# Performance work log

Measured on AMD Instinct MI355X. Metric: run time of the kernel, lower is better.

The kernel has to match this reference:

```python
import jax, jax.numpy as jnp
import numpy as np

H = 768   # config.hidden_size
B = 1024  # batch
S = 256   # attention context length
C1, C2, C3 = 202, 183, 11  # num_class for crit, law, time


def setup_inputs() -> dict:
    key = jax.random.key(0)
    ks = jax.random.split(key, 18)
    sd = 1.0 / np.sqrt(H)
    def u(k, shape):
        return jax.random.uniform(k, shape, jnp.float32, -sd, sd)
    return {
        "x": jax.random.normal(ks[0], (B, H), jnp.float32),
        "attn": jax.random.normal(ks[1], (B, S, H), jnp.float32),
        # 3 LSTMCells (tasks crit, law, time), stacked
        "Wih": u(ks[2], (3, 4 * H, H)),
        "Whh": u(ks[3], (3, 4 * H, H)),
        "bih": u(ks[4], (3, 4 * H)),
        "bhh": u(ks[5], (3, 4 * H)),
        # edge (2->3) hidden/cell state Linear (only edge whose FC is reached)
        "hfc_W": u(ks[6], (H, H)), "hfc_b": u(ks[7], (H,)),
        "cfc_W": u(ks[8], (H, H)), "cfc_b": u(ks[9], (H,)),
        # midfc per task
        "midfc_W": u(ks[10], (3, H, H)), "midfc_b": u(ks[11], (3, H)),
        # outfc per task (distinct class counts)
        "out1_W": u(ks[12], (C1, H)), "out1_b": u(ks[13], (C1,)),
        "out2_W": u(ks[14], (C2, H)), "out2_b": u(ks[15], (C2,)),
        "out3_W": u(ks[16], (C3, H)), "out3_b": u(ks[17], (C3,)),
    }


def _lstm_cell(x, h, c, Wih, Whh, bih, bhh):
    # torch nn.LSTMCell: gate order i, f, g, o
    gates = x @ Wih.T + bih + h @ Whh.T + bhh
    i, f, g, o = jnp.split(gates, 4, axis=-1)
    c_new = jax.nn.sigmoid(f) * c + jax.nn.sigmoid(i) * jnp.tanh(g)
    h_new = jax.nn.sigmoid(o) * jnp.tanh(c_new)
    return h_new, c_new


def _attend(h, attn):
    # Attention: ratio = softmax(bmm(attn, h)); result = bmm(attn^T, ratio)
    w = jax.nn.softmax(jnp.einsum('bsh,bh->bs', attn, h), axis=1)
    return jnp.einsum('bsh,bs->bh', attn, w)


def _head(h, mW, mb, oW, ob):
    # more_fc=True: outfc(relu(midfc(h)))
    return jax.nn.relu(h @ mW.T + mb) @ oW.T + ob


def reference(x, attn, Wih, Whh, bih, bhh, hfc_W, hfc_b, cfc_W, cfc_b,
              midfc_W, midfc_b, out1_W, out1_b, out2_W, out2_b, out3_W, out3_b):
    # graph "[(1 2),(1 3),(2 3)]": edges 1->2, 1->3, 2->3; initial hidden_list all zero.
    z = jnp.zeros_like(x)
    # task 1 (crit): runs on zero state; first-touch sets hidden[2]=hidden[3]=(h1,c1)
    h1, c1 = _lstm_cell(x, z, z, Wih[0], Whh[0], bih[0], bhh[0])
    # task 2 (law): state = (h1, c1)
    h2, c2 = _lstm_cell(x, h1, c1, Wih[1], Whh[1], bih[1], bhh[1])
    # edge 2->3 applies the per-edge Linear and accumulates into hidden[3]
    hp3 = h1 + h2 @ hfc_W.T + hfc_b
    cp3 = c1 + c2 @ cfc_W.T + cfc_b
    # task 3 (time)
    h3, c3 = _lstm_cell(x, hp3, cp3, Wih[2], Whh[2], bih[2], bhh[2])
    # attention over encoder context, per task head
    a1 = _attend(h1, attn)
    a2 = _attend(h2, attn)
    a3 = _attend(h3, attn)
    o1 = _head(a1, midfc_W[0], midfc_b[0], out1_W, out1_b)
    o2 = _head(a2, midfc_W[1], midfc_b[1], out2_W, out2_b)
    o3 = _head(a3, midfc_W[2], midfc_b[2], out3_W, out3_b)
    return (o1, o2, o3)
```

## Files before the change

kernel.cpp:

```cpp
#include <hip/hip_runtime.h>


typedef unsigned short u16;
typedef _Float16       f16x8 __attribute__((ext_vector_type(8)));
typedef float          f32x4 __attribute__((ext_vector_type(4)));

#define SWZ(r) ((((r) + ((r) >> 2))) & 3)
#define VMCNT(N) asm volatile("s_waitcnt vmcnt(" #N ")" ::: "memory")
#define KBAR()  do { __builtin_amdgcn_s_barrier(); __builtin_amdgcn_sched_barrier(0); } while (0)

__device__ __forceinline__ u16 f2h(float f) {
  _Float16 h = (_Float16)f;
  return __builtin_bit_cast(u16, h);
}
__device__ __forceinline__ float sigm(float x) { return 1.f / (1.f + __expf(-x)); }
__device__ __forceinline__ float ftanh(float x) { return 1.f - 2.f / (__expf(2.f * x) + 1.f); }

__device__ __forceinline__ void gld16(const u16* g, u16* l) {
  __builtin_amdgcn_global_load_lds(
      (const __attribute__((address_space(1))) unsigned int*)(g),
      (__attribute__((address_space(3))) unsigned int*)(l),
      16, 0, 0);
}

struct KP { const u16 *pA1, *pA2, *pW1_0, *pW2_0, *pW1_1, *pW2_1; };

__device__ __forceinline__ void stage_tile(const KP& kp, int kt, int ntA,
                                           u16* Asb, u16* Bsb, int wv) {
  const bool s1 = (kt < ntA);
  const int off = (s1 ? kt : kt - ntA) * 32;
  gld16((s1 ? kp.pA1  : kp.pA2 ) + off, Asb + wv * 512);
  gld16((s1 ? kp.pW1_0 : kp.pW2_0) + off, Bsb + wv * 512);
  gld16((s1 ? kp.pW1_1 : kp.pW2_1) + off, Bsb + 2048 + wv * 512);
}

__device__ __forceinline__ void compute_tile(const u16* Asb, const u16* Bsb,
                                             int wv, int frow, int fsl, f32x4* acc) {
  const int ar = wv * 16 + frow;
  f16x8 ah = *(const f16x8*)(Asb + ar * 32 + ((fsl ^ SWZ(ar)) * 8));
  f16x8 bh[8];
#pragma unroll
  for (int n = 0; n < 8; ++n) {
    const int br = n * 16 + frow;
    bh[n] = *(const f16x8*)(Bsb + br * 32 + ((fsl ^ SWZ(br)) * 8));
  }
#pragma unroll
  for (int n = 0; n < 8; ++n)
    acc[n] = __builtin_amdgcn_mfma_f32_16x16x32_f16(ah, bh[n], acc[n], 0, 0, 0);
}

#define KLOOP(kp, ntA, NT, As, Bs, wv, frow, fsl, acc)                          \
  do {                                                                          \
    stage_tile(kp, 0, ntA, As, Bs, wv);                                         \
    stage_tile(kp, 1, ntA, As + 2048, Bs + 4096, wv);                           \
    stage_tile(kp, 2, ntA, As + 4096, Bs + 8192, wv);                           \
    for (int t = 0; t < NT - 2; ++t) {                                          \
      VMCNT(6); KBAR();                                                         \
      const int cb = t & 3;                                                     \
      compute_tile(As + cb * 2048, Bs + cb * 4096, wv, frow, fsl, acc);         \
      if (t + 3 < NT) {                                                         \
        const int sb = (t + 3) & 3;                                             \
        stage_tile(kp, t + 3, ntA, As + sb * 2048, Bs + sb * 4096, wv);         \
      }                                                                         \
    }                                                                           \
    VMCNT(3); KBAR();                                                           \
    compute_tile(As + ((NT - 2) & 3) * 2048, Bs + ((NT - 2) & 3) * 4096,        \
                 wv, frow, fsl, acc);                                           \
    VMCNT(0); KBAR();                                                           \
    compute_tile(As + ((NT - 1) & 3) * 2048, Bs + ((NT - 1) & 3) * 4096,        \
                 wv, frow, fsl, acc);                                           \
  } while (0)

struct GJob {
  const u16* A; const u16* W;
  float* outf; u16* outh;
  const float* bias; const float* bias2; const float* addend;
  int N; int ldc; int relu;
};
struct GArgs { GJob j[3]; };

__global__ __launch_bounds__(256)
void gemm_k(GArgs P)
{
  const GJob jb = P.j[blockIdx.z];
  const int bn0 = blockIdx.x * 128;
  if (bn0 >= jb.N) return;
  const int bm0 = blockIdx.y * 64;

  __shared__ __align__(16) u16 As[4 * 64 * 32];
  __shared__ __align__(16) u16 Bs[4 * 128 * 32];

  const int tid = threadIdx.x, lane = tid & 63, wv = tid >> 6;
  const int frow = lane & 15, fsl = lane >> 4;

  const int ra  = tid >> 2,        csa  = (tid & 3) ^ SWZ(ra);
  const int rb0 = tid >> 2,        csb0 = (tid & 3) ^ SWZ(rb0);
  const int rb1 = (tid >> 2) + 64, csb1 = (tid & 3) ^ SWZ(rb1);
  int wr0 = bn0 + rb0; if (wr0 >= jb.N) wr0 = jb.N - 1;
  int wr1 = bn0 + rb1; if (wr1 >= jb.N) wr1 = jb.N - 1;

  KP kp;
  kp.pA1 = kp.pA2 = jb.A + (size_t)(bm0 + ra) * 768 + csa * 8;
  kp.pW1_0 = kp.pW2_0 = jb.W + (size_t)wr0 * 768 + csb0 * 8;
  kp.pW1_1 = kp.pW2_1 = jb.W + (size_t)wr1 * 768 + csb1 * 8;

  f32x4 acc[8];
#pragma unroll
  for (int n = 0; n < 8; ++n) acc[n] = (f32x4){0.f, 0.f, 0.f, 0.f};

  KLOOP(kp, 24, 24, As, Bs, wv, frow, fsl, acc);

  const int rb = (lane >> 4) * 4;
  const int cc = lane & 15;
#pragma unroll
  for (int n = 0; n < 8; ++n) {
    const int col = bn0 + n * 16 + cc;
    if (col >= jb.N) continue;
    float bv = 0.f;
    if (jb.bias)  bv += jb.bias[col];
    if (jb.bias2) bv += jb.bias2[col];
    const int row0 = bm0 + wv * 16 + rb;
#pragma unroll
    for (int r = 0; r < 4; ++r) {
      const int row = row0 + r;
      float v = acc[n][r] + bv;
      if (jb.addend) v += jb.addend[(size_t)row * jb.ldc + col];
      if (jb.relu)   v = fmaxf(v, 0.f);
      if (jb.outf)   jb.outf[(size_t)row * jb.ldc + col] = v;
      if (jb.outh)   jb.outh[(size_t)row * jb.ldc + col] = f2h(v);
    }
  }
}

__global__ __launch_bounds__(256)
void cell_k(const u16* __restrict__ A1, const u16* __restrict__ A2,
            const u16* __restrict__ W1, const u16* __restrict__ W2,
            const float* __restrict__ bi, const float* __restrict__ bh_,
            const float* __restrict__ cprev,
            float* __restrict__ hf, float* __restrict__ cf,
            u16* __restrict__ hh, u16* __restrict__ ch, int NT)
{
  const int bj0 = blockIdx.x * 32;
  const int bm0 = blockIdx.y * 64;

  __shared__ __align__(16) u16 As[4 * 64 * 32];
  __shared__ __align__(16) u16 Bs[4 * 128 * 32];

  const int tid = threadIdx.x, lane = tid & 63, wv = tid >> 6;
  const int frow = lane & 15, fsl = lane >> 4;

  const int ra  = tid >> 2,        csa  = (tid & 3) ^ SWZ(ra);
  const int rb0 = tid >> 2,        csb0 = (tid & 3) ^ SWZ(rb0);
  const int rb1 = (tid >> 2) + 64, csb1 = (tid & 3) ^ SWZ(rb1);
  const int wr0 = (rb0 >> 5) * 768 + bj0 + (rb0 & 31);
  const int wr1 = (rb1 >> 5) * 768 + bj0 + (rb1 & 31);

  KP kp;
  kp.pA1  = A1 + (size_t)(bm0 + ra) * 768 + csa * 8;
  kp.pA2  = A2 + (size_t)(bm0 + ra) * 768 + csa * 8;
  kp.pW1_0 = W1 + (size_t)wr0 * 768 + csb0 * 8;
  kp.pW2_0 = W2 + (size_t)wr0 * 768 + csb0 * 8;
  kp.pW1_1 = W1 + (size_t)wr1 * 768 + csb1 * 8;
  kp.pW2_1 = W2 + (size_t)wr1 * 768 + csb1 * 8;

  f32x4 acc[8];
#pragma unroll
  for (int n = 0; n < 8; ++n) acc[n] = (f32x4){0.f, 0.f, 0.f, 0.f};

  KLOOP(kp, 24, NT, As, Bs, wv, frow, fsl, acc);

  const int rb = (lane >> 4) * 4;
  const int cc = lane & 15;
#pragma unroll
  for (int jj = 0; jj < 2; ++jj) {
    const int j = bj0 + jj * 16 + cc;
    const float b_i = bi[j]        + bh_[j];
    const float b_f = bi[768 + j]  + bh_[768 + j];
    const float b_g = bi[1536 + j] + bh_[1536 + j];
    const float b_o = bi[2304 + j] + bh_[2304 + j];
    const int row0 = bm0 + wv * 16 + rb;
#pragma unroll
    for (int r = 0; r < 4; ++r) {
      const int row = row0 + r;
      float gi = acc[0 + jj][r] + b_i;
      float gf = acc[2 + jj][r] + b_f;
      float gg = acc[4 + jj][r] + b_g;
      float go = acc[6 + jj][r] + b_o;
      float c = sigm(gi) * ftanh(gg);
      if (cprev) c += sigm(gf) * cprev[row * 768 + j];
      float h = sigm(go) * ftanh(c);
      if (hf) hf[row * 768 + j] = h;
      if (cf) cf[row * 768 + j] = c;
      if (hh) hh[row * 768 + j] = f2h(h);
      if (ch) ch[row * 768 + j] = f2h(c);
    }
  }
}

struct CvtArgs {
  const float* src[9];
  u16*         dst[9];
  int n[9];
  int pfx[10];
};

__global__ __launch_bounds__(256)
void cvt_k(CvtArgs a)
{
  int blk = blockIdx.x, s = 0;
  while (s < 8 && blk >= a.pfx[s + 1]) ++s;
  int idx = ((blk - a.pfx[s]) * 256 + (int)threadIdx.x) * 4;
  if (idx >= a.n[s]) return;
  float4 v = *(const float4*)(a.src[s] + idx);
  ushort4 h;
  h.x = f2h(v.x); h.y = f2h(v.y); h.z = f2h(v.z); h.w = f2h(v.w);
  *(ushort4*)(a.dst[s] + idx) = h;
}

__global__ __launch_bounds__(256)
void attn_k(const float* __restrict__ attn,
            const float* __restrict__ h1, const float* __restrict__ h2,
            const float* __restrict__ h3,
            u16* __restrict__ a1, u16* __restrict__ a2, u16* __restrict__ a3)
{
  const int b = blockIdx.x, tid = threadIdx.x;
  const int lane = tid & 63, wv = tid >> 6;
  __shared__ float accW[4][3][768];
  __shared__ float lsumW[4][3];

  const float* ab = attn + (size_t)b * 256 * 768;
  const int cb = lane * 4;

  float4 hh[3][3];
#pragma unroll
  for (int j = 0; j < 3; ++j) {
    hh[0][j] = *(const float4*)(h1 + b * 768 + j * 256 + cb);
    hh[1][j] = *(const float4*)(h2 + b * 768 + j * 256 + cb);
    hh[2][j] = *(const float4*)(h3 + b * 768 + j * 256 + cb);
  }

  float4 acc[3][3];
#pragma unroll
  for (int t3 = 0; t3 < 3; ++t3)
#pragma unroll
    for (int j = 0; j < 3; ++j) acc[t3][j] = (float4){0.f, 0.f, 0.f, 0.f};
  float lsum[3] = {0.f, 0.f, 0.f};

  const int row0 = wv * 64;
  for (int sub = 0; sub < 16; ++sub) {
    const float* rp = ab + (size_t)(row0 + sub * 4) * 768 + cb;
    float4 vv[4][3];
#pragma unroll
    for (int s = 0; s < 4; ++s)
#pragma unroll
      for (int j = 0; j < 3; ++j)
        vv[s][j] = *(const float4*)(rp + s * 768 + j * 256);

    float q[3][4];
#pragma unroll
    for (int t3 = 0; t3 < 3; ++t3)
#pragma unroll
      for (int s = 0; s < 4; ++s) {
        float d = 0.f;
#pragma unroll
        for (int j = 0; j < 3; ++j) {
          d = fmaf(vv[s][j].x, hh[t3][j].x, d);
          d = fmaf(vv[s][j].y, hh[t3][j].y, d);
          d = fmaf(vv[s][j].z, hh[t3][j].z, d);
          d = fmaf(vv[s][j].w, hh[t3][j].w, d);
        }
        q[t3][s] = d;
      }
#pragma unroll
    for (int t3 = 0; t3 < 3; ++t3)
#pragma unroll
      for (int s = 0; s < 4; ++s) {
#pragma unroll
        for (int d = 1; d < 64; d <<= 1)
          q[t3][s] += __shfl_xor(q[t3][s], d);
        q[t3][s] = __expf(q[t3][s]);
      }
#pragma unroll
    for (int t3 = 0; t3 < 3; ++t3)
#pragma unroll
      for (int s = 0; s < 4; ++s) {
        const float p = q[t3][s];
        lsum[t3] += p;
#pragma unroll
        for (int j = 0; j < 3; ++j) {
          acc[t3][j].x = fmaf(p, vv[s][j].x, acc[t3][j].x);
          acc[t3][j].y = fmaf(p, vv[s][j].y, acc[t3][j].y);
          acc[t3][j].z = fmaf(p, vv[s][j].z, acc[t3][j].z);
          acc[t3][j].w = fmaf(p, vv[s][j].w, acc[t3][j].w);
        }
      }
  }

#pragma unroll
  for (int t3 = 0; t3 < 3; ++t3)
#pragma unroll
    for (int j = 0; j < 3; ++j)
      *(float4*)(&accW[wv][t3][j * 256 + cb]) = acc[t3][j];
  if (lane == 0) {
#pragma unroll
    for (int t3 = 0; t3 < 3; ++t3) lsumW[wv][t3] = lsum[t3];
  }
  __syncthreads();

  float ltot[3];
#pragma unroll
  for (int t3 = 0; t3 < 3; ++t3)
    ltot[t3] = lsumW[0][t3] + lsumW[1][t3] + lsumW[2][t3] + lsumW[3][t3];
  u16* outs[3] = { a1, a2, a3 };
#pragma unroll
  for (int cc = 0; cc < 3; ++cc) {
    const int c = tid + cc * 256;
#pragma unroll
    for (int t3 = 0; t3 < 3; ++t3) {
      float s = accW[0][t3][c] + accW[1][t3][c] + accW[2][t3][c] + accW[3][t3][c];
      outs[t3][b * 768 + c] = f2h(s / ltot[t3]);
    }
  }
}

extern "C" void kernel_launch(void* const* d_in, const int* in_sizes, int n_in,
                              void* d_out, int out_size, void* d_ws, size_t ws_size,
                              hipStream_t stream)
{
  const float* x    = (const float*)d_in[0];
  const float* attn = (const float*)d_in[1];
  const float* Wih  = (const float*)d_in[2];
  const float* Whh  = (const float*)d_in[3];
  const float* bih  = (const float*)d_in[4];
  const float* bhh  = (const float*)d_in[5];
  const float* hfcW = (const float*)d_in[6];
  const float* hfcb = (const float*)d_in[7];
  const float* cfcW = (const float*)d_in[8];
  const float* cfcb = (const float*)d_in[9];
  const float* midW = (const float*)d_in[10];
  const float* midb = (const float*)d_in[11];
  const float* o1W  = (const float*)d_in[12];
  const float* o1b  = (const float*)d_in[13];
  const float* o2W  = (const float*)d_in[14];
  const float* o2b  = (const float*)d_in[15];
  const float* o3W  = (const float*)d_in[16];
  const float* o3b  = (const float*)d_in[17];
  float* out = (float*)d_out;
  char*  ws  = (char*)d_ws;

  float* h1f  = (float*)(ws + 0);
  float* c1f  = (float*)(ws + 3145728);
  float* h2f  = (float*)(ws + 6291456);
  float* cp3f = (float*)(ws + 9437184);
  float* h3f  = (float*)(ws + 12582912);
  u16*   xh   = (u16*)(ws + 15728640);
  u16*   Wihh = (u16*)(ws + 17301504);
  u16*   Whhh = (u16*)(ws + 31457280);
  u16*   hfch = (u16*)(ws + 40894464);
  u16*   cfch = (u16*)(ws + 42074112);
  u16*   midh = (u16*)(ws + 43253760);
  u16*   o1h  = (u16*)(ws + 46792704);
  u16*   o2h  = (u16*)(ws + 47102976);
  u16*   o3h  = (u16*)(ws + 47384064);
  u16*   h1h  = (u16*)(ws + 47400960);
  u16*   h2h  = (u16*)(ws + 48973824);
  u16*   c2h  = (u16*)(ws + 50546688);
  u16*   hp3h = (u16*)(ws + 52119552);
  u16*   a1h  = (u16*)(ws + 53692416);
  u16*   a2h  = (u16*)(ws + 55265280);
  u16*   a3h  = (u16*)(ws + 56838144);
  u16*   m1h  = (u16*)(ws + 58411008);
  u16*   m2h  = (u16*)(ws + 59983872);
  u16*   m3h  = (u16*)(ws + 61556736);

  CvtArgs ca;
  const float* srcs[9] = { x, Wih, Whh + 2359296, hfcW, cfcW, midW, o1W, o2W, o3W };
  u16*         dsts[9] = { xh, Wihh, Whhh, hfch, cfch, midh, o1h, o2h, o3h };
  int ns[9] = { 786432, 7077888, 4718592, 589824, 589824, 1769472, 155136, 140544, 8448 };
  int pfx = 0;
  for (int i = 0; i < 9; ++i) {
    ca.src[i] = srcs[i]; ca.dst[i] = dsts[i]; ca.n[i] = ns[i];
    ca.pfx[i] = pfx; pfx += (ns[i] + 1023) / 1024;
  }
  ca.pfx[9] = pfx;
  cvt_k<<<pfx, 256, 0, stream>>>(ca);

  GArgs P;

  cell_k<<<dim3(24, 16), 256, 0, stream>>>(xh, xh, Wihh, Wihh,
      bih, bhh, nullptr, h1f, c1f, h1h, nullptr, 24);

  cell_k<<<dim3(24, 16), 256, 0, stream>>>(xh, h1h,
      Wihh + (size_t)3072 * 768, Whhh,
      bih + 3072, bhh + 3072, c1f, h2f, nullptr, h2h, c2h, 48);

  P = GArgs{};
  P.j[0] = { h2h, hfch, nullptr, hp3h, hfcb, nullptr, h1f, 768, 768, 0 };
  P.j[1] = { c2h, cfch, cp3f, nullptr, cfcb, nullptr, c1f, 768, 768, 0 };
  gemm_k<<<dim3(6, 16, 2), 256, 0, stream>>>(P);

  cell_k<<<dim3(24, 16), 256, 0, stream>>>(xh, hp3h,
      Wihh + (size_t)6144 * 768, Whhh + 2359296,
      bih + 6144, bhh + 6144, cp3f, h3f, nullptr, nullptr, nullptr, 48);

  attn_k<<<1024, 256, 0, stream>>>(attn, h1f, h2f, h3f, a1h, a2h, a3h);

  P = GArgs{};
  P.j[0] = { a1h, midh,           nullptr, m1h, midb,        nullptr, nullptr, 768, 768, 1 };
  P.j[1] = { a2h, midh +  589824, nullptr, m2h, midb +  768, nullptr, nullptr, 768, 768, 1 };
  P.j[2] = { a3h, midh + 1179648, nullptr, m3h, midb + 1536, nullptr, nullptr, 768, 768, 1 };
  gemm_k<<<dim3(6, 16, 3), 256, 0, stream>>>(P);

  P = GArgs{};
  P.j[0] = { m1h, o1h, out,          nullptr, o1b, nullptr, nullptr, 202, 202, 0 };
  P.j[1] = { m2h, o2h, out + 206848, nullptr, o2b, nullptr, nullptr, 183, 183, 0 };
  P.j[2] = { m3h, o3h, out + 394240, nullptr, o3b, nullptr, nullptr,  11,  11, 0 };
  gemm_k<<<dim3(2, 16, 3), 256, 0, stream>>>(P);

  (void)in_sizes; (void)n_in; (void)out_size; (void)ws_size;
}
```

Measured before the change: 323.1 us.

## Fuse all stages into one persistent kernel with software grid barriers

Replaces the eight separate kernel launches (convert, three LSTM cells, edge GEMMs, attention, midfc, outfc) with a single persistent kernel of 512 blocks that moves between stages through an atomic-counter grid barrier. The goal is to remove per-launch overhead and the tail drain at each kernel boundary. The cost is that some stages leave many blocks idle (for example 96 or 192 of 512 active), and each barrier adds atomic and spin-wait latency. Correctness depends on all 512 blocks being resident at once, which the launch bounds of 2 blocks per CU are meant to allow.

Result: slower. 819.7 us (+153.7%).

```diff
diff --git a/kernel.cpp b/kernel.cpp
--- a/kernel.cpp
+++ b/kernel.cpp
@@ -5,6 +5,7 @@
 typedef _Float16       f16x8 __attribute__((ext_vector_type(8)));
 typedef float          f32x4 __attribute__((ext_vector_type(4)));
 
+#define NBLK 512u
 #define SWZ(r) ((((r) + ((r) >> 2))) & 3)
 #define VMCNT(N) asm volatile("s_waitcnt vmcnt(" #N ")" ::: "memory")
 #define KBAR()  do { __builtin_amdgcn_s_barrier(); __builtin_amdgcn_sched_barrier(0); } while (0)
@@ -23,13 +24,31 @@
       16, 0, 0);
 }
 
+__device__ __forceinline__ void gbar(unsigned* bar, int tid) {
+  __syncthreads();
+  if (tid == 0) {
+    __threadfence();
+    unsigned g = __hip_atomic_load(bar + 1, __ATOMIC_RELAXED, __HIP_MEMORY_SCOPE_AGENT);
+    unsigned a = __hip_atomic_fetch_add(bar, 1u, __ATOMIC_ACQ_REL, __HIP_MEMORY_SCOPE_AGENT);
+    if (a == NBLK - 1u) {
+      __hip_atomic_store(bar, 0u, __ATOMIC_RELAXED, __HIP_MEMORY_SCOPE_AGENT);
+      __hip_atomic_fetch_add(bar + 1, 1u, __ATOMIC_RELEASE, __HIP_MEMORY_SCOPE_AGENT);
+    } else {
+      while (__hip_atomic_load(bar + 1, __ATOMIC_RELAXED, __HIP_MEMORY_SCOPE_AGENT) == g)
+        __builtin_amdgcn_s_sleep(2);
+    }
+    __threadfence();
+  }
+  __syncthreads();
+}
+
 struct KP { const u16 *pA1, *pA2, *pW1_0, *pW2_0, *pW1_1, *pW2_1; };
 
 __device__ __forceinline__ void stage_tile(const KP& kp, int kt, int ntA,
                                            u16* Asb, u16* Bsb, int wv) {
   const bool s1 = (kt < ntA);
   const int off = (s1 ? kt : kt - ntA) * 32;
-  gld16((s1 ? kp.pA1  : kp.pA2 ) + off, Asb + wv * 512);
+  gld16((s1 ? kp.pA1   : kp.pA2  ) + off, Asb + wv * 512);
   gld16((s1 ? kp.pW1_0 : kp.pW2_0) + off, Bsb + wv * 512);
   gld16((s1 ? kp.pW1_1 : kp.pW2_1) + off, Bsb + 2048 + wv * 512);
 }
@@ -49,27 +68,28 @@
     acc[n] = __builtin_amdgcn_mfma_f32_16x16x32_f16(ah, bh[n], acc[n], 0, 0, 0);
 }
 
-#define KLOOP(kp, ntA, NT, As, Bs, wv, frow, fsl, acc)                          \
-  do {                                                                          \
-    stage_tile(kp, 0, ntA, As, Bs, wv);                                         \
-    stage_tile(kp, 1, ntA, As + 2048, Bs + 4096, wv);                           \
-    stage_tile(kp, 2, ntA, As + 4096, Bs + 8192, wv);                           \
-    for (int t = 0; t < NT - 2; ++t) {                                          \
-      VMCNT(6); KBAR();                                                         \
-      const int cb = t & 3;                                                     \
-      compute_tile(As + cb * 2048, Bs + cb * 4096, wv, frow, fsl, acc);         \
-      if (t + 3 < NT) {                                                         \
-        const int sb = (t + 3) & 3;                                             \
-        stage_tile(kp, t + 3, ntA, As + sb * 2048, Bs + sb * 4096, wv);         \
-      }                                                                         \
-    }                                                                           \
-    VMCNT(3); KBAR();                                                           \
-    compute_tile(As + ((NT - 2) & 3) * 2048, Bs + ((NT - 2) & 3) * 4096,        \
-                 wv, frow, fsl, acc);                                           \
-    VMCNT(0); KBAR();                                                           \
-    compute_tile(As + ((NT - 1) & 3) * 2048, Bs + ((NT - 1) & 3) * 4096,        \
-                 wv, frow, fsl, acc);                                           \
-  } while (0)
+__device__ __forceinline__ void kloop4(const KP& kp, int ntA, int NT,
+                                       u16* As, u16* Bs,
+                                       int wv, int frow, int fsl, f32x4* acc) {
+  stage_tile(kp, 0, ntA, As,        Bs,        wv);
+  stage_tile(kp, 1, ntA, As + 2048, Bs + 4096, wv);
+  stage_tile(kp, 2, ntA, As + 4096, Bs + 8192, wv);
+  for (int t = 0; t < NT - 2; ++t) {
+    VMCNT(6); KBAR();
+    const int cb = t & 3;
+    compute_tile(As + cb * 2048, Bs + cb * 4096, wv, frow, fsl, acc);
+    if (t + 3 < NT) {
+      const int sb = (t + 3) & 3;
+      stage_tile(kp, t + 3, ntA, As + sb * 2048, Bs + sb * 4096, wv);
+    }
+  }
+  VMCNT(3); KBAR();
+  compute_tile(As + ((NT - 2) & 3) * 2048, Bs + ((NT - 2) & 3) * 4096,
+               wv, frow, fsl, acc);
+  VMCNT(0); KBAR();
+  compute_tile(As + ((NT - 1) & 3) * 2048, Bs + ((NT - 1) & 3) * 4096,
+               wv, frow, fsl, acc);
+}
 
 struct GJob {
   const u16* A; const u16* W;
@@ -77,38 +97,30 @@
   const float* bias; const float* bias2; const float* addend;
   int N; int ldc; int relu;
 };
-struct GArgs { GJob j[3]; };
-
-__global__ __launch_bounds__(256)
-void gemm_k(GArgs P)
-{
-  const GJob jb = P.j[blockIdx.z];
-  const int bn0 = blockIdx.x * 128;
+
+__device__ __forceinline__ void run_gemm(const GJob& jb, int bx, int by,
+                                         u16* As, u16* Bs, int tid) {
+  const int bn0 = bx * 128;
   if (bn0 >= jb.N) return;
-  const int bm0 = blockIdx.y * 64;
-
-  __shared__ __align__(16) u16 As[4 * 64 * 32];
-  __shared__ __align__(16) u16 Bs[4 * 128 * 32];
-
-  const int tid = threadIdx.x, lane = tid & 63, wv = tid >> 6;
+  const int bm0 = by * 64;
+  const int lane = tid & 63, wv = tid >> 6;
   const int frow = lane & 15, fsl = lane >> 4;
 
   const int ra  = tid >> 2,        csa  = (tid & 3) ^ SWZ(ra);
-  const int rb0 = tid >> 2,        csb0 = (tid & 3) ^ SWZ(rb0);
   const int rb1 = (tid >> 2) + 64, csb1 = (tid & 3) ^ SWZ(rb1);
-  int wr0 = bn0 + rb0; if (wr0 >= jb.N) wr0 = jb.N - 1;
+  int wr0 = bn0 + ra;  if (wr0 >= jb.N) wr0 = jb.N - 1;
   int wr1 = bn0 + rb1; if (wr1 >= jb.N) wr1 = jb.N - 1;
 
   KP kp;
   kp.pA1 = kp.pA2 = jb.A + (size_t)(bm0 + ra) * 768 + csa * 8;
-  kp.pW1_0 = kp.pW2_0 = jb.W + (size_t)wr0 * 768 + csb0 * 8;
+  kp.pW1_0 = kp.pW2_0 = jb.W + (size_t)wr0 * 768 + csa * 8;
   kp.pW1_1 = kp.pW2_1 = jb.W + (size_t)wr1 * 768 + csb1 * 8;
 
   f32x4 acc[8];
 #pragma unroll
   for (int n = 0; n < 8; ++n) acc[n] = (f32x4){0.f, 0.f, 0.f, 0.f};
 
-  KLOOP(kp, 24, 24, As, Bs, wv, frow, fsl, acc);
+  kloop4(kp, 24, 24, As, Bs, wv, frow, fsl, acc);
 
   const int rb = (lane >> 4) * 4;
   const int cc = lane & 15;
@@ -132,34 +144,28 @@
   }
 }
 
-__global__ __launch_bounds__(256)
-void cell_k(const u16* __restrict__ A1, const u16* __restrict__ A2,
-            const u16* __restrict__ W1, const u16* __restrict__ W2,
-            const float* __restrict__ bi, const float* __restrict__ bh_,
-            const float* __restrict__ cprev,
-            float* __restrict__ hf, float* __restrict__ cf,
-            u16* __restrict__ hh, u16* __restrict__ ch, int NT)
-{
-  const int bj0 = blockIdx.x * 32;
-  const int bm0 = blockIdx.y * 64;
-
-  __shared__ __align__(16) u16 As[4 * 64 * 32];
-  __shared__ __align__(16) u16 Bs[4 * 128 * 32];
-
-  const int tid = threadIdx.x, lane = tid & 63, wv = tid >> 6;
+__device__ __forceinline__ void run_cell(const u16* A1, const u16* A2,
+                                         const u16* W1, const u16* W2,
+                                         const float* bi, const float* bh_,
+                                         const float* cprev,
+                                         float* hf, float* cf, u16* hh, u16* ch,
+                                         int NT, int bx, int by,
+                                         u16* As, u16* Bs, int tid) {
+  const int bj0 = bx * 32;
+  const int bm0 = by * 64;
+  const int lane = tid & 63, wv = tid >> 6;
   const int frow = lane & 15, fsl = lane >> 4;
 
   const int ra  = tid >> 2,        csa  = (tid & 3) ^ SWZ(ra);
-  const int rb0 = tid >> 2,        csb0 = (tid & 3) ^ SWZ(rb0);
   const int rb1 = (tid >> 2) + 64, csb1 = (tid & 3) ^ SWZ(rb1);
-  const int wr0 = (rb0 >> 5) * 768 + bj0 + (rb0 & 31);
+  const int wr0 = (ra >> 5) * 768 + bj0 + (ra & 31);
   const int wr1 = (rb1 >> 5) * 768 + bj0 + (rb1 & 31);
 
   KP kp;
   kp.pA1  = A1 + (size_t)(bm0 + ra) * 768 + csa * 8;
   kp.pA2  = A2 + (size_t)(bm0 + ra) * 768 + csa * 8;
-  kp.pW1_0 = W1 + (size_t)wr0 * 768 + csb0 * 8;
-  kp.pW2_0 = W2 + (size_t)wr0 * 768 + csb0 * 8;
+  kp.pW1_0 = W1 + (size_t)wr0 * 768 + csa * 8;
+  kp.pW2_0 = W2 + (size_t)wr0 * 768 + csa * 8;
   kp.pW1_1 = W1 + (size_t)wr1 * 768 + csb1 * 8;
   kp.pW2_1 = W2 + (size_t)wr1 * 768 + csb1 * 8;
 
@@ -167,7 +173,7 @@
 #pragma unroll
   for (int n = 0; n < 8; ++n) acc[n] = (f32x4){0.f, 0.f, 0.f, 0.f};
 
-  KLOOP(kp, 24, NT, As, Bs, wv, frow, fsl, acc);
+  kloop4(kp, 24, NT, As, Bs, wv, frow, fsl, acc);
 
   const int rb = (lane >> 4) * 4;
   const int cc = lane & 15;
@@ -197,129 +203,201 @@
   }
 }
 
-struct CvtArgs {
-  const float* src[9];
-  u16*         dst[9];
-  int n[9];
-  int pfx[10];
+__device__ __forceinline__ void cvt_seg(const float* s, u16* d, int n4,
+                                        int gtid, int nthr) {
+  for (int i = gtid; i < n4; i += nthr) {
+    float4 v = ((const float4*)s)[i];
+    ushort4 h;
+    h.x = f2h(v.x); h.y = f2h(v.y); h.z = f2h(v.z); h.w = f2h(v.w);
+    ((ushort4*)d)[i] = h;
+  }
+}
+
+struct MP {
+  const float *x, *attn, *Wih, *Whh, *bih, *bhh, *hfcW, *hfcb, *cfcW, *cfcb;
+  const float *midW, *midb, *o1W, *o1b, *o2W, *o2b, *o3W, *o3b;
+  float* out;
+  float *h1f, *c1f, *h2f, *cp3f, *h3f;
+  u16 *xh, *Wihh, *Whhh, *hfch, *cfch, *midh, *o1h, *o2h, *o3h;
+  u16 *h1h, *h2h, *c2h, *hp3h, *a1h, *a2h, *a3h, *m1h, *m2h, *m3h;
+  unsigned* bar;
 };
 
-__global__ __launch_bounds__(256)
-void cvt_k(CvtArgs a)
+__global__ __launch_bounds__(256, 2)
+void mega_k(MP p)
 {
-  int blk = blockIdx.x, s = 0;
-  while (s < 8 && blk >= a.pfx[s + 1]) ++s;
-  int idx = ((blk - a.pfx[s]) * 256 + (int)threadIdx.x) * 4;
-  if (idx >= a.n[s]) return;
-  float4 v = *(const float4*)(a.src[s] + idx);
-  ushort4 h;
-  h.x = f2h(v.x); h.y = f2h(v.y); h.z = f2h(v.z); h.w = f2h(v.w);
-  *(ushort4*)(a.dst[s] + idx) = h;
-}
-
-__global__ __launch_bounds__(256)
-void attn_k(const float* __restrict__ attn,
-            const float* __restrict__ h1, const float* __restrict__ h2,
-            const float* __restrict__ h3,
-            u16* __restrict__ a1, u16* __restrict__ a2, u16* __restrict__ a3)
-{
-  const int b = blockIdx.x, tid = threadIdx.x;
+  __shared__ __align__(16) char smem[49152];
+  u16* As = (u16*)smem;
+  u16* Bs = (u16*)(smem + 16384);
+  float* accW  = (float*)smem;
+  float* lsumW = (float*)(smem + 36864);
+
+  const int blk = blockIdx.x, tid = threadIdx.x;
   const int lane = tid & 63, wv = tid >> 6;
-  __shared__ float accW[4][3][768];
-  __shared__ float lsumW[4][3];
-
-  const float* ab = attn + (size_t)b * 256 * 768;
-  const int cb = lane * 4;
-
-  float4 hh[3][3];
-#pragma unroll
-  for (int j = 0; j < 3; ++j) {
-    hh[0][j] = *(const float4*)(h1 + b * 768 + j * 256 + cb);
-    hh[1][j] = *(const float4*)(h2 + b * 768 + j * 256 + cb);
-    hh[2][j] = *(const float4*)(h3 + b * 768 + j * 256 + cb);
-  }
-
-  float4 acc[3][3];
-#pragma unroll
-  for (int t3 = 0; t3 < 3; ++t3)
-#pragma unroll
-    for (int j = 0; j < 3; ++j) acc[t3][j] = (float4){0.f, 0.f, 0.f, 0.f};
-  float lsum[3] = {0.f, 0.f, 0.f};
-
-  const int row0 = wv * 64;
-  for (int sub = 0; sub < 16; ++sub) {
-    const float* rp = ab + (size_t)(row0 + sub * 4) * 768 + cb;
-    float4 vv[4][3];
-#pragma unroll
-    for (int s = 0; s < 4; ++s)
+
+  {
+    const int g = blk * 256 + tid, N = NBLK * 256;
+    cvt_seg(p.x,             p.xh,             196608,  g, N);
+    cvt_seg(p.Wih,           p.Wihh,           1769472, g, N);
+    cvt_seg(p.Whh + 2359296, p.Whhh,           1179648, g, N);
+    cvt_seg(p.hfcW,          p.hfch,           147456,  g, N);
+    cvt_seg(p.cfcW,          p.cfch,           147456,  g, N);
+    cvt_seg(p.midW,          p.midh,           442368,  g, N);
+    cvt_seg(p.o1W,           p.o1h,            38784,   g, N);
+    cvt_seg(p.o2W,           p.o2h,            35136,   g, N);
+    cvt_seg(p.o3W,           p.o3h,            2112,    g, N);
+  }
+  gbar(p.bar, tid);
+
+  if (blk < 384) {
+    run_cell(p.xh, p.xh, p.Wihh, p.Wihh, p.bih, p.bhh, nullptr,
+             p.h1f, p.c1f, p.h1h, nullptr, 24, blk % 24, blk / 24, As, Bs, tid);
+  }
+  gbar(p.bar, tid);
+
+  if (blk < 384) {
+    run_cell(p.xh, p.h1h, p.Wihh + (size_t)3072 * 768, p.Whhh,
+             p.bih + 3072, p.bhh + 3072, p.c1f,
+             p.h2f, nullptr, p.h2h, p.c2h, 48, blk % 24, blk / 24, As, Bs, tid);
+  }
+  gbar(p.bar, tid);
+
+  if (blk < 192) {
+    const int job = blk / 96, r = blk % 96;
+    GJob jb;
+    if (job == 0) jb = { p.h2h, p.hfch, nullptr, p.hp3h, p.hfcb, nullptr, p.h1f, 768, 768, 0 };
+    else          jb = { p.c2h, p.cfch, p.cp3f, nullptr, p.cfcb, nullptr, p.c1f, 768, 768, 0 };
+    run_gemm(jb, r % 6, r / 6, As, Bs, tid);
+  }
+  gbar(p.bar, tid);
+
+  if (blk < 384) {
+    run_cell(p.xh, p.hp3h, p.Wihh + (size_t)6144 * 768, p.Whhh + 2359296,
+             p.bih + 6144, p.bhh + 6144, p.cp3f,
+             p.h3f, nullptr, nullptr, nullptr, 48, blk % 24, blk / 24, As, Bs, tid);
+  }
+  gbar(p.bar, tid);
+
+  for (int rep = 0; rep < 2; ++rep) {
+    const int b = blk + rep * NBLK;
+    const float* ab = p.attn + (size_t)b * 196608;
+    const int cb = lane * 4;
+
+    __syncthreads();
+
+    float4 hh[3][3];
+#pragma unroll
+    for (int j = 0; j < 3; ++j) {
+      hh[0][j] = *(const float4*)(p.h1f + b * 768 + j * 256 + cb);
+      hh[1][j] = *(const float4*)(p.h2f + b * 768 + j * 256 + cb);
+      hh[2][j] = *(const float4*)(p.h3f + b * 768 + j * 256 + cb);
+    }
+    float4 acc[3][3];
+#pragma unroll
+    for (int t3 = 0; t3 < 3; ++t3)
+#pragma unroll
+      for (int j = 0; j < 3; ++j) acc[t3][j] = (float4){0.f, 0.f, 0.f, 0.f};
+    float lsum[3] = {0.f, 0.f, 0.f};
+
+    const int row0 = wv * 64;
+    for (int sub = 0; sub < 16; ++sub) {
+      const float* rp = ab + (size_t)(row0 + sub * 4) * 768 + cb;
+      float4 vv[4][3];
+#pragma unroll
+      for (int s = 0; s < 4; ++s)
+#pragma unroll
+        for (int j = 0; j < 3; ++j)
+          vv[s][j] = *(const float4*)(rp + s * 768 + j * 256);
+
+      float q[3][4];
+#pragma unroll
+      for (int t3 = 0; t3 < 3; ++t3)
+#pragma unroll
+        for (int s = 0; s < 4; ++s) {
+          float d = 0.f;
+#pragma unroll
+          for (int j = 0; j < 3; ++j) {
+            d = fmaf(vv[s][j].x, hh[t3][j].x, d);
+            d = fmaf(vv[s][j].y, hh[t3][j].y, d);
+            d = fmaf(vv[s][j].z, hh[t3][j].z, d);
+            d = fmaf(vv[s][j].w, hh[t3][j].w, d);
+          }
+          q[t3][s] = d;
+        }
+#pragma unroll
+      for (int t3 = 0; t3 < 3; ++t3)
+#pragma unroll
+        for (int s = 0; s < 4; ++s) {
+#pragma unroll
+          for (int d = 1; d < 64; d <<= 1)
+            q[t3][s] += __shfl_xor(q[t3][s], d);
+          q[t3][s] = __expf(q[t3][s]);
+        }
+#pragma unroll
+      for (int t3 = 0; t3 < 3; ++t3)
+#pragma unroll
+        for (int s = 0; s < 4; ++s) {
+          const float pw = q[t3][s];
+          lsum[t3] += pw;
+#pragma unroll
+          for (int j = 0; j < 3; ++j) {
+            acc[t3][j].x = fmaf(pw, vv[s][j].x, acc[t3][j].x);
+            acc[t3][j].y = fmaf(pw, vv[s][j].y, acc[t3][j].y);
+            acc[t3][j].z = fmaf(pw, vv[s][j].z, acc[t3][j].z);
+            acc[t3][j].w = fmaf(pw, vv[s][j].w, acc[t3][j].w);
+          }
+        }
+    }
+
+    __syncthreads();
+#pragma unroll
+    for (int t3 = 0; t3 < 3; ++t3)
 #pragma unroll
       for (int j = 0; j < 3; ++j)
-        vv[s][j] = *(const float4*)(rp + s * 768 + j * 256);
-
-    float q[3][4];
+        *(float4*)(&accW[(wv * 3 + t3) * 768 + j * 256 + cb]) = acc[t3][j];
+    if (lane == 0) {
+#pragma unroll
+      for (int t3 = 0; t3 < 3; ++t3) lsumW[wv * 3 + t3] = lsum[t3];
+    }
+    __syncthreads();
+
+    float ltot[3];
 #pragma unroll
     for (int t3 = 0; t3 < 3; ++t3)
-#pragma unroll
-      for (int s = 0; s < 4; ++s) {
-        float d = 0.f;
-#pragma unroll
-        for (int j = 0; j < 3; ++j) {
-          d = fmaf(vv[s][j].x, hh[t3][j].x, d);
-          d = fmaf(vv[s][j].y, hh[t3][j].y, d);
-          d = fmaf(vv[s][j].z, hh[t3][j].z, d);
-          d = fmaf(vv[s][j].w, hh[t3][j].w, d);
-        }
-        q[t3][s] = d;
+      ltot[t3] = lsumW[t3] + lsumW[3 + t3] + lsumW[6 + t3] + lsumW[9 + t3];
+    u16* outs[3] = { p.a1h, p.a2h, p.a3h };
+#pragma unroll
+    for (int cc = 0; cc < 3; ++cc) {
+      const int c = tid + cc * 256;
+#pragma unroll
+      for (int t3 = 0; t3 < 3; ++t3) {
+        float s = accW[t3 * 768 + c] + accW[(3 + t3) * 768 + c] +
+                  accW[(6 + t3) * 768 + c] + accW[(9 + t3) * 768 + c];
+        outs[t3][b * 768 + c] = f2h(s / ltot[t3]);
       }
-#pragma unroll
-    for (int t3 = 0; t3 < 3; ++t3)
-#pragma unroll
-      for (int s = 0; s < 4; ++s) {
-#pragma unroll
-        for (int d = 1; d < 64; d <<= 1)
-          q[t3][s] += __shfl_xor(q[t3][s], d);
-        q[t3][s] = __expf(q[t3][s]);
-      }
-#pragma unroll
-    for (int t3 = 0; t3 < 3; ++t3)
-#pragma unroll
-      for (int s = 0; s < 4; ++s) {
-        const float p = q[t3][s];
-        lsum[t3] += p;
-#pragma unroll
-        for (int j = 0; j < 3; ++j) {
-          acc[t3][j].x = fmaf(p, vv[s][j].x, acc[t3][j].x);
-          acc[t3][j].y = fmaf(p, vv[s][j].y, acc[t3][j].y);
-          acc[t3][j].z = fmaf(p, vv[s][j].z, acc[t3][j].z);
-          acc[t3][j].w = fmaf(p, vv[s][j].w, acc[t3][j].w);
-        }
-      }
-  }
-
-#pragma unroll
-  for (int t3 = 0; t3 < 3; ++t3)
-#pragma unroll
-    for (int j = 0; j < 3; ++j)
-      *(float4*)(&accW[wv][t3][j * 256 + cb]) = acc[t3][j];
-  if (lane == 0) {
-#pragma unroll
-    for (int t3 = 0; t3 < 3; ++t3) lsumW[wv][t3] = lsum[t3];
-  }
-  __syncthreads();
-
-  float ltot[3];
-#pragma unroll
-  for (int t3 = 0; t3 < 3; ++t3)
-    ltot[t3] = lsumW[0][t3] + lsumW[1][t3] + lsumW[2][t3] + lsumW[3][t3];
-  u16* outs[3] = { a1, a2, a3 };
-#pragma unroll
-  for (int cc = 0; cc < 3; ++cc) {
-    const int c = tid + cc * 256;
-#pragma unroll
-    for (int t3 = 0; t3 < 3; ++t3) {
-      float s = accW[0][t3][c] + accW[1][t3][c] + accW[2][t3][c] + accW[3][t3][c];
-      outs[t3][b * 768 + c] = f2h(s / ltot[t3]);
-    }
+    }
+  }
+  gbar(p.bar, tid);
+
+  if (blk < 288) {
+    const int t = blk / 96, r = blk % 96;
+    const u16* a = (t == 0) ? p.a1h : (t == 1) ? p.a2h : p.a3h;
+    u16*       m = (t == 0) ? p.m1h : (t == 1) ? p.m2h : p.m3h;
+    GJob jb = { a, p.midh + (size_t)t * 589824, nullptr, m,
+                p.midb + t * 768, nullptr, nullptr, 768, 768, 1 };
+    run_gemm(jb, r % 6, r / 6, As, Bs, tid);
+  }
+  gbar(p.bar, tid);
+
+  if (blk < 96) {
+    const int t = blk / 32, r = blk % 32;
+    const u16* m = (t == 0) ? p.m1h : (t == 1) ? p.m2h : p.m3h;
+    const u16* w = (t == 0) ? p.o1h : (t == 1) ? p.o2h : p.o3h;
+    const float* bb = (t == 0) ? p.o1b : (t == 1) ? p.o2b : p.o3b;
+    float* o = p.out + ((t == 0) ? 0 : (t == 1) ? 206848 : 394240);
+    const int N = (t == 0) ? 202 : (t == 1) ? 183 : 11;
+    GJob jb = { m, w, o, nullptr, bb, nullptr, nullptr, N, N, 0 };
+    run_gemm(jb, r % 2, r / 2, As, Bs, tid);
   }
 }
 
@@ -327,95 +405,57 @@
                               void* d_out, int out_size, void* d_ws, size_t ws_size,
                               hipStream_t stream)
 {
-  const float* x    = (const float*)d_in[0];
-  const float* attn = (const float*)d_in[1];
-  const float* Wih  = (const float*)d_in[2];
-  const float* Whh  = (const float*)d_in[3];
-  const float* bih  = (const float*)d_in[4];
-  const float* bhh  = (const float*)d_in[5];
-  const float* hfcW = (const float*)d_in[6];
-  const float* hfcb = (const float*)d_in[7];
-  const float* cfcW = (const float*)d_in[8];
-  const float* cfcb = (const float*)d_in[9];
-  const float* midW = (const float*)d_in[10];
-  const float* midb = (const float*)d_in[11];
-  const float* o1W  = (const float*)d_in[12];
-  const float* o1b  = (const float*)d_in[13];
-  const float* o2W  = (const float*)d_in[14];
-  const float* o2b  = (const float*)d_in[15];
-  const float* o3W  = (const float*)d_in[16];
-  const float* o3b  = (const float*)d_in[17];
-  float* out = (float*)d_out;
-  char*  ws  = (char*)d_ws;
-
-  float* h1f  = (float*)(ws + 0);
-  float* c1f  = (float*)(ws + 3145728);
-  float* h2f  = (float*)(ws + 6291456);
-  float* cp3f = (float*)(ws + 9437184);
-  float* h3f  = (float*)(ws + 12582912);
-  u16*   xh   = (u16*)(ws + 15728640);
-  u16*   Wihh = (u16*)(ws + 17301504);
-  u16*   Whhh = (u16*)(ws + 31457280);
-  u16*   hfch = (u16*)(ws + 40894464);
-  u16*   cfch = (u16*)(ws + 42074112);
-  u16*   midh = (u16*)(ws + 43253760);
-  u16*   o1h  = (u16*)(ws + 46792704);
-  u16*   o2h  = (u16*)(ws + 47102976);
-  u16*   o3h  = (u16*)(ws + 47384064);
-  u16*   h1h  = (u16*)(ws + 47400960);
-  u16*   h2h  = (u16*)(ws + 48973824);
-  u16*   c2h  = (u16*)(ws + 50546688);
-  u16*   hp3h = (u16*)(ws + 52119552);
-  u16*   a1h  = (u16*)(ws + 53692416);
-  u16*   a2h  = (u16*)(ws + 55265280);
-  u16*   a3h  = (u16*)(ws + 56838144);
-  u16*   m1h  = (u16*)(ws + 58411008);
-  u16*   m2h  = (u16*)(ws + 59983872);
-  u16*   m3h  = (u16*)(ws + 61556736);
-
-  CvtArgs ca;
-  const float* srcs[9] = { x, Wih, Whh + 2359296, hfcW, cfcW, midW, o1W, o2W, o3W };
-  u16*         dsts[9] = { xh, Wihh, Whhh, hfch, cfch, midh, o1h, o2h, o3h };
-  int ns[9] = { 786432, 7077888, 4718592, 589824, 589824, 1769472, 155136, 140544, 8448 };
-  int pfx = 0;
-  for (int i = 0; i < 9; ++i) {
-    ca.src[i] = srcs[i]; ca.dst[i] = dsts[i]; ca.n[i] = ns[i];
-    ca.pfx[i] = pfx; pfx += (ns[i] + 1023) / 1024;
-  }
-  ca.pfx[9] = pfx;
-  cvt_k<<<pfx, 256, 0, stream>>>(ca);
-
-  GArgs P;
-
-  cell_k<<<dim3(24, 16), 256, 0, stream>>>(xh, xh, Wihh, Wihh,
-      bih, bhh, nullptr, h1f, c1f, h1h, nullptr, 24);
-
-  cell_k<<<dim3(24, 16), 256, 0, stream>>>(xh, h1h,
-      Wihh + (size_t)3072 * 768, Whhh,
-      bih + 3072, bhh + 3072, c1f, h2f, nullptr, h2h, c2h, 48);
-
-  P = GArgs{};
-  P.j[0] = { h2h, hfch, nullptr, hp3h, hfcb, nullptr, h1f, 768, 768, 0 };
-  P.j[1] = { c2h, cfch, cp3f, nullptr, cfcb, nullptr, c1f, 768, 768, 0 };
-  gemm_k<<<dim3(6, 16, 2), 256, 0, stream>>>(P);
-
-  cell_k<<<dim3(24, 16), 256, 0, stream>>>(xh, hp3h,
-      Wihh + (size_t)6144 * 768, Whhh + 2359296,
-      bih + 6144, bhh + 6144, cp3f, h3f, nullptr, nullptr, nullptr, 48);
-
-  attn_k<<<1024, 256, 0, stream>>>(attn, h1f, h2f, h3f, a1h, a2h, a3h);
-
-  P = GArgs{};
-  P.j[0] = { a1h, midh,           nullptr, m1h, midb,        nullptr, nullptr, 768, 768, 1 };
-  P.j[1] = { a2h, midh +  589824, nullptr, m2h, midb +  768, nullptr, nullptr, 768, 768, 1 };
-  P.j[2] = { a3h, midh + 1179648, nullptr, m3h, midb + 1536, nullptr, nullptr, 768, 768, 1 };
-  gemm_k<<<dim3(6, 16, 3), 256, 0, stream>>>(P);
-
-  P = GArgs{};
-  P.j[0] = { m1h, o1h, out,          nullptr, o1b, nullptr, nullptr, 202, 202, 0 };
-  P.j[1] = { m2h, o2h, out + 206848, nullptr, o2b, nullptr, nullptr, 183, 183, 0 };
-  P.j[2] = { m3h, o3h, out + 394240, nullptr, o3b, nullptr, nullptr,  11,  11, 0 };
-  gemm_k<<<dim3(2, 16, 3), 256, 0, stream>>>(P);
+  char* ws = (char*)d_ws;
+
+  MP p;
+  p.x    = (const float*)d_in[0];
+  p.attn = (const float*)d_in[1];
+  p.Wih  = (const float*)d_in[2];
+  p.Whh  = (const float*)d_in[3];
+  p.bih  = (const float*)d_in[4];
+  p.bhh  = (const float*)d_in[5];
+  p.hfcW = (const float*)d_in[6];
+  p.hfcb = (const float*)d_in[7];
+  p.cfcW = (const float*)d_in[8];
+  p.cfcb = (const float*)d_in[9];
+  p.midW = (const float*)d_in[10];
+  p.midb = (const float*)d_in[11];
+  p.o1W  = (const float*)d_in[12];
+  p.o1b  = (const float*)d_in[13];
+  p.o2W  = (const float*)d_in[14];
+  p.o2b  = (const float*)d_in[15];
+  p.o3W  = (const float*)d_in[16];
+  p.o3b  = (const float*)d_in[17];
+  p.out  = (float*)d_out;
+
+  p.h1f  = (float*)(ws + 0);
+  p.c1f  = (float*)(ws + 3145728);
+  p.h2f  = (float*)(ws + 6291456);
+  p.cp3f = (float*)(ws + 9437184);
+  p.h3f  = (float*)(ws + 12582912);
+  p.xh   = (u16*)(ws + 15728640);
+  p.Wihh = (u16*)(ws + 17301504);
+  p.Whhh = (u16*)(ws + 31457280);
+  p.hfch = (u16*)(ws + 40894464);
+  p.cfch = (u16*)(ws + 42074112);
+  p.midh = (u16*)(ws + 43253760);
+  p.o1h  = (u16*)(ws + 46792704);
+  p.o2h  = (u16*)(ws + 47102976);
+  p.o3h  = (u16*)(ws + 47384064);
+  p.h1h  = (u16*)(ws + 47400960);
+  p.h2h  = (u16*)(ws + 48973824);
+  p.c2h  = (u16*)(ws + 50546688);
+  p.hp3h = (u16*)(ws + 52119552);
+  p.a1h  = (u16*)(ws + 53692416);
+  p.a2h  = (u16*)(ws + 55265280);
+  p.a3h  = (u16*)(ws + 56838144);
+  p.m1h  = (u16*)(ws + 58411008);
+  p.m2h  = (u16*)(ws + 59983872);
+  p.m3h  = (u16*)(ws + 61556736);
+  p.bar  = (unsigned*)(ws + 63129600);
+
+  hipMemsetAsync(p.bar, 0, 16, stream);
+  mega_k<<<dim3(NBLK), dim3(256), 0, stream>>>(p);
 
   (void)in_sizes; (void)n_in; (void)out_size; (void)ws_size;
 }
```
